# Optimization experiments

Measured on AMD Instinct MI355X. Metric: run time of the kernel, lower is better.

## Reference

```python
import jax, jax.numpy as jnp
import numpy as np
import math

D_MODEL = 1024
NUM_HEADS = 16
D_K = D_MODEL // NUM_HEADS
SEQ = 4096
THETA = 10000.0


def _rope_tables(d_k, max_seq_len, theta):
    freqs = 1.0 / theta ** (jnp.arange(0, d_k, 2, dtype=jnp.float32) / d_k)  # (d_k/2,)
    pos = jnp.arange(max_seq_len, dtype=jnp.float32)
    ang = pos[:, None] * freqs[None, :]  # (S, d_k/2)
    return jnp.cos(ang), jnp.sin(ang)


def setup_inputs() -> dict:
    key = jax.random.key(0)
    ks = jax.random.split(key, 5)
    std = math.sqrt(2.0 / (D_MODEL + D_MODEL))
    def trunc_w(k):
        return jax.random.truncated_normal(k, -3.0, 3.0, (D_MODEL, D_MODEL), jnp.float32) * std
    x = jax.random.normal(ks[0], (1, SEQ, D_MODEL), jnp.float32)
    Wq, Wk, Wv, Wo = trunc_w(ks[1]), trunc_w(ks[2]), trunc_w(ks[3]), trunc_w(ks[4])
    cos, sin = _rope_tables(D_K, SEQ, THETA)
    positions = jnp.arange(SEQ, dtype=jnp.int32)
    return {"x": x, "Wq": Wq, "Wk": Wk, "Wv": Wv, "Wo": Wo,
            "cos": cos, "sin": sin, "positions": positions}


def _apply_rope(t, cos, sin, positions):
    # t: (b, h, s, d_k); cos/sin: (max_s, d_k/2)
    c = cos[positions][None, None]  # (1,1,s,d_k/2)
    s = sin[positions][None, None]
    x1, x2 = t[..., ::2], t[..., 1::2]
    rotated = jnp.stack([x1 * c - x2 * s, x1 * s + x2 * c], axis=-1)  # (b,h,s,d_k/2,2)
    return rotated.reshape(t.shape)


def reference(x, Wq, Wk, Wv, Wo, cos, sin, positions):
    b, s, d = x.shape
    h, dk = NUM_HEADS, D_K
    def proj(W):
        y = jnp.einsum('bsi,oi->bso', x, W)
        return y.reshape(b, s, h, dk).transpose(0, 2, 1, 3)  # (b,h,s,dk)
    Q, K, V = proj(Wq), proj(Wk), proj(Wv)
    Q = _apply_rope(Q, cos, sin, positions)
    K = _apply_rope(K, cos, sin, positions)
    scores = jnp.einsum('bhqd,bhkd->bhqk', Q, K) / math.sqrt(dk)
    causal = jnp.tril(jnp.ones((s, s), dtype=bool))
    scores = jnp.where(causal[None, None], scores, -jnp.inf)
    weights = jax.nn.softmax(scores, axis=-1)
    y = jnp.einsum('bhqk,bhkd->bhqd', weights, V)
    y = y.transpose(0, 2, 1, 3).reshape(b, s, d)
    return jnp.einsum('bsi,oi->bso', y, Wo)
```

## Files before the change

### kernel.cpp

```cpp
#include <hip/hip_runtime.h>
#include <math.h>

#define SEQ 4096
#define DM  1024
#define NH  16
#define DK  64

typedef __attribute__((ext_vector_type(4))) float f32x4;
typedef __attribute__((ext_vector_type(8))) short bf16x8;
typedef __attribute__((ext_vector_type(8))) unsigned short u16x8;

__device__ __forceinline__ unsigned short bf_hi(float f) {
    return (unsigned short)(__float_as_uint(f) >> 16);
}
__device__ __forceinline__ float bf_f(unsigned short s) {
    return __uint_as_float(((unsigned)s) << 16);
}

union FragU { u16x8 u; bf16x8 b; ushort4 q[2]; };

template<int MODE>
__global__ __launch_bounds__(256)
void gemm_mfma(const float* __restrict__ A,
               const float* __restrict__ W0, const float* __restrict__ W1,
               const float* __restrict__ W2,
               unsigned short* __restrict__ OQh, unsigned short* __restrict__ OQl,
               unsigned short* __restrict__ OKh, unsigned short* __restrict__ OKl,
               unsigned short* __restrict__ OVh, unsigned short* __restrict__ OVl,
               float* __restrict__ Ofp,
               const float* __restrict__ cosT, const float* __restrict__ sinT,
               const int* __restrict__ positions)
{
    constexpr int NT = (MODE == 4) ? 48 : 16;
    __shared__ unsigned short As[128][72];
    __shared__ unsigned short Bs[64][72];

    const int t   = threadIdx.x;
    const int bid = blockIdx.x;
    const int q8  = (32 * NT) >> 3;
    const int swz = (bid & 7) * q8 + (bid >> 3);
    const int by  = swz / NT;
    const int bxf = swz % NT;
    const int wt  = (MODE == 4) ? (bxf >> 4) : 0;
    const int bx  = (MODE == 4) ? (bxf & 15) : bxf;
    const int m0  = by * 128;
    const int n0  = bx * 64;
    const float* W = (MODE == 4) ? (wt == 0 ? W0 : (wt == 1 ? W1 : W2)) : W0;

    const int lane = t & 63;
    const int w    = t >> 6;
    const int wr   = w >> 1, wc = w & 1;
    const int l15  = lane & 15;
    const int lg   = lane >> 4;

    const int ar = t >> 1, ah = t & 1;
    const int br = t >> 2, bq = t & 3;
    const float* Ap = &A[(size_t)(m0 + ar) * DM + ah * 16];
    const float* Wp = &W[(size_t)(n0 + br) * DM + bq * 8];

    f32x4 acc[4][2];
#pragma unroll
    for (int mi = 0; mi < 4; ++mi)
#pragma unroll
        for (int ni = 0; ni < 2; ++ni) acc[mi][ni] = (f32x4){0.f, 0.f, 0.f, 0.f};

    float4 pa[4], pb[2];
#pragma unroll
    for (int u = 0; u < 4; ++u) pa[u] = *reinterpret_cast<const float4*>(Ap + u * 4);
    pb[0] = *reinterpret_cast<const float4*>(Wp);
    pb[1] = *reinterpret_cast<const float4*>(Wp + 4);

    for (int kt = 0; kt < 32; ++kt) {
#pragma unroll
        for (int g = 0; g < 4; ++g) {
            ushort4 hv, lv;
            const float4 v = pa[g];
            const float vf[4] = {v.x, v.y, v.z, v.w};
            unsigned short* hp = (unsigned short*)&hv;
            unsigned short* lp = (unsigned short*)&lv;
#pragma unroll
            for (int jj = 0; jj < 4; ++jj) {
                const unsigned short h = bf_hi(vf[jj]);
                hp[jj] = h; lp[jj] = bf_hi(vf[jj] - bf_f(h));
            }
            *reinterpret_cast<ushort4*>(&As[ar][8 * g + 4 * ah])      = hv;
            *reinterpret_cast<ushort4*>(&As[ar][32 + 8 * g + 4 * ah]) = lv;
        }
#pragma unroll
        for (int u = 0; u < 2; ++u) {
            const int g = 2 * (bq & 1) + u, h2 = bq >> 1;
            ushort4 hv, lv;
            const float4 v = pb[u];
            const float vf[4] = {v.x, v.y, v.z, v.w};
            unsigned short* hp = (unsigned short*)&hv;
            unsigned short* lp = (unsigned short*)&lv;
#pragma unroll
            for (int jj = 0; jj < 4; ++jj) {
                const unsigned short h = bf_hi(vf[jj]);
                hp[jj] = h; lp[jj] = bf_hi(vf[jj] - bf_f(h));
            }
            *reinterpret_cast<ushort4*>(&Bs[br][8 * g + 4 * h2])      = hv;
            *reinterpret_cast<ushort4*>(&Bs[br][32 + 8 * g + 4 * h2]) = lv;
        }
        __syncthreads();

        if (kt < 31) {
            const float* Apn = Ap + (kt + 1) * 32;
            const float* Wpn = Wp + (kt + 1) * 32;
#pragma unroll
            for (int u = 0; u < 4; ++u) pa[u] = *reinterpret_cast<const float4*>(Apn + u * 4);
            pb[0] = *reinterpret_cast<const float4*>(Wpn);
            pb[1] = *reinterpret_cast<const float4*>(Wpn + 4);
        }

        FragU a_h[4], a_l[4], b_h[2], b_l[2];
#pragma unroll
        for (int mi = 0; mi < 4; ++mi) {
            const int row = wr * 64 + mi * 16 + l15;
            a_h[mi].u = *reinterpret_cast<const u16x8*>(&As[row][8 * lg]);
            a_l[mi].u = *reinterpret_cast<const u16x8*>(&As[row][32 + 8 * lg]);
        }
#pragma unroll
        for (int ni = 0; ni < 2; ++ni) {
            const int row = wc * 32 + ni * 16 + l15;
            b_h[ni].u = *reinterpret_cast<const u16x8*>(&Bs[row][8 * lg]);
            b_l[ni].u = *reinterpret_cast<const u16x8*>(&Bs[row][32 + 8 * lg]);
        }
#pragma unroll
        for (int mi = 0; mi < 4; ++mi)
#pragma unroll
            for (int ni = 0; ni < 2; ++ni) {
                f32x4 c = acc[mi][ni];
                c = __builtin_amdgcn_mfma_f32_16x16x32_bf16(a_h[mi].b, b_h[ni].b, c, 0, 0, 0);
                c = __builtin_amdgcn_mfma_f32_16x16x32_bf16(a_h[mi].b, b_l[ni].b, c, 0, 0, 0);
                c = __builtin_amdgcn_mfma_f32_16x16x32_bf16(a_l[mi].b, b_h[ni].b, c, 0, 0, 0);
                acc[mi][ni] = c;
            }
        __syncthreads();
    }

    if (MODE == 0) {
#pragma unroll
        for (int mi = 0; mi < 4; ++mi)
#pragma unroll
            for (int ni = 0; ni < 2; ++ni)
#pragma unroll
                for (int r = 0; r < 4; ++r) {
                    const int m  = m0 + wr * 64 + mi * 16 + lg * 4 + r;
                    const int ng = n0 + wc * 32 + ni * 16 + l15;
                    Ofp[(size_t)m * DM + ng] = acc[mi][ni][r];
                }
    } else if (wt == 2) {
#pragma unroll
        for (int mi = 0; mi < 4; ++mi)
#pragma unroll
            for (int ni = 0; ni < 2; ++ni) {
                ushort4 hv, lv;
                unsigned short* hp = (unsigned short*)&hv;
                unsigned short* lp = (unsigned short*)&lv;
#pragma unroll
                for (int r = 0; r < 4; ++r) {
                    const float f = acc[mi][ni][r];
                    const unsigned short h = bf_hi(f);
                    hp[r] = h; lp[r] = bf_hi(f - bf_f(h));
                }
                const int ng = n0 + wc * 32 + ni * 16 + l15;
                const size_t off = (size_t)ng * SEQ + m0 + wr * 64 + mi * 16 + lg * 4;
                *reinterpret_cast<ushort4*>(&OVh[off]) = hv;
                *reinterpret_cast<ushort4*>(&OVl[off]) = lv;
            }
    } else {
        unsigned short* Oh = (wt == 0) ? OQh : OKh;
        unsigned short* Ol = (wt == 0) ? OQl : OKl;
        const int head = bx;
#pragma unroll
        for (int mi = 0; mi < 4; ++mi)
#pragma unroll
            for (int r = 0; r < 4; ++r) {
                const int m   = m0 + wr * 64 + mi * 16 + lg * 4 + r;
                const int pos = positions[m];
#pragma unroll
                for (int ni = 0; ni < 2; ++ni) {
                    float val = acc[mi][ni][r];
                    const int d = wc * 32 + ni * 16 + l15;
                    const float other = __shfl_xor(val, 1);
                    const float cc = cosT[pos * (DK / 2) + (d >> 1)];
                    const float ss = sinT[pos * (DK / 2) + (d >> 1)];
                    val = (d & 1) ? fmaf(other, ss, val * cc)
                                  : fmaf(other, -ss, val * cc);
                    if (wt == 0) val *= 0.125f;
                    const unsigned short h = bf_hi(val);
                    const unsigned short l = bf_hi(val - bf_f(h));
                    const size_t off = ((size_t)head * SEQ + m) * DK + d;
                    Oh[off] = h; Ol[off] = l;
                }
            }
    }
}

__global__ __launch_bounds__(256)
void attn_mfma(const unsigned short* __restrict__ Qhi, const unsigned short* __restrict__ Qlo,
               const unsigned short* __restrict__ Khi, const unsigned short* __restrict__ Klo,
               const unsigned short* __restrict__ Vhi, const unsigned short* __restrict__ Vlo,
               float* __restrict__ Y)
{
    __shared__ unsigned short KsH[64][68], KsL[64][68];
    __shared__ unsigned short VsH[64][68], VsL[64][68];

    const int t    = threadIdx.x;
    const int lane = t & 63;
    const int w    = t >> 6;
    const int bid  = blockIdx.x;
    const int h    = 2 * (bid & 7) + ((bid >> 3) >> 5);
    const int bx   = (bid >> 3) & 31;

    const int l15 = lane & 15;
    const int lg  = lane >> 4;
    const int dg  = lg * 4;

#pragma unroll 1
    for (int pass = 0; pass < 2; ++pass) {
        const int qt = pass ? (63 - bx) : bx;

        bf16x8 qh[2], ql[2];
        {
            const size_t qrow = ((size_t)h * SEQ + (size_t)qt * 64 + w * 16 + l15) * DK;
#pragma unroll
            for (int c = 0; c < 2; ++c) {
                FragU uh, ul;
                uh.q[0] = *reinterpret_cast<const ushort4*>(&Qhi[qrow + c * 32 + dg]);
                uh.q[1] = *reinterpret_cast<const ushort4*>(&Qhi[qrow + c * 32 + 16 + dg]);
                ul.q[0] = *reinterpret_cast<const ushort4*>(&Qlo[qrow + c * 32 + dg]);
                ul.q[1] = *reinterpret_cast<const ushort4*>(&Qlo[qrow + c * 32 + 16 + dg]);
                qh[c] = uh.b; ql[c] = ul.b;
            }
        }

        f32x4 yacc[4];
#pragma unroll
        for (int dt = 0; dt < 4; ++dt) yacc[dt] = (f32x4){0.f, 0.f, 0.f, 0.f};
        float m_run = -1e30f, l_run = 0.0f;

        for (int kt = 0; kt <= qt; ++kt) {
            __syncthreads();
            {
                const int srow = t >> 3;
                const int scol = (t & 7) * 8;
#pragma unroll
                for (int u = 0; u < 2; ++u) {
                    const int row = u * 32 + srow;
                    const size_t gK = ((size_t)h * SEQ + (size_t)kt * 64 + row) * DK + scol;
                    const size_t gV = ((size_t)h * DK + row) * SEQ + (size_t)kt * 64 + scol;
                    FragU a;
                    a.u = *reinterpret_cast<const u16x8*>(&Khi[gK]);
                    *reinterpret_cast<ushort4*>(&KsH[row][scol])     = a.q[0];
                    *reinterpret_cast<ushort4*>(&KsH[row][scol + 4]) = a.q[1];
                    a.u = *reinterpret_cast<const u16x8*>(&Klo[gK]);
                    *reinterpret_cast<ushort4*>(&KsL[row][scol])     = a.q[0];
                    *reinterpret_cast<ushort4*>(&KsL[row][scol + 4]) = a.q[1];
                    a.u = *reinterpret_cast<const u16x8*>(&Vhi[gV]);
                    *reinterpret_cast<ushort4*>(&VsH[row][scol])     = a.q[0];
                    *reinterpret_cast<ushort4*>(&VsH[row][scol + 4]) = a.q[1];
                    a.u = *reinterpret_cast<const u16x8*>(&Vlo[gV]);
                    *reinterpret_cast<ushort4*>(&VsL[row][scol])     = a.q[0];
                    *reinterpret_cast<ushort4*>(&VsL[row][scol + 4]) = a.q[1];
                }
            }
            __syncthreads();

            const bool diag = (kt == qt);

            f32x4 st[4];
            __builtin_amdgcn_s_setprio(1);
#pragma unroll
            for (int ktile = 0; ktile < 4; ++ktile) {
                if (diag && ktile > w) {
                    st[ktile] = (f32x4){-1e30f, -1e30f, -1e30f, -1e30f};
                    continue;
                }
                f32x4 s = (f32x4){0.f, 0.f, 0.f, 0.f};
#pragma unroll
                for (int c = 0; c < 2; ++c) {
                    const int d0 = c * 32 + dg;
                    FragU ahf, alf;
                    ahf.q[0] = *reinterpret_cast<const ushort4*>(&KsH[ktile * 16 + l15][d0]);
                    ahf.q[1] = *reinterpret_cast<const ushort4*>(&KsH[ktile * 16 + l15][d0 + 16]);
                    alf.q[0] = *reinterpret_cast<const ushort4*>(&KsL[ktile * 16 + l15][d0]);
                    alf.q[1] = *reinterpret_cast<const ushort4*>(&KsL[ktile * 16 + l15][d0 + 16]);
                    s = __builtin_amdgcn_mfma_f32_16x16x32_bf16(ahf.b, qh[c], s, 0, 0, 0);
                    s = __builtin_amdgcn_mfma_f32_16x16x32_bf16(ahf.b, ql[c], s, 0, 0, 0);
                    s = __builtin_amdgcn_mfma_f32_16x16x32_bf16(alf.b, qh[c], s, 0, 0, 0);
                }
                st[ktile] = s;
            }
            __builtin_amdgcn_s_setprio(0);

            if (diag) {
                const int qrel = w * 16 + l15;
#pragma unroll
                for (int ktile = 0; ktile < 4; ++ktile)
#pragma unroll
                    for (int r = 0; r < 4; ++r)
                        if (ktile * 16 + dg + r > qrel) st[ktile][r] = -1e30f;
            }

            float rowmax = -1e30f;
#pragma unroll
            for (int ktile = 0; ktile < 4; ++ktile)
#pragma unroll
                for (int r = 0; r < 4; ++r) rowmax = fmaxf(rowmax, st[ktile][r]);
            rowmax = fmaxf(rowmax, __shfl_xor(rowmax, 16));
            rowmax = fmaxf(rowmax, __shfl_xor(rowmax, 32));
            if (!__all(rowmax <= m_run + 8.0f)) {
                const float mnew   = fmaxf(m_run, rowmax);
                const float factor = __expf(m_run - mnew);
                l_run *= factor;
#pragma unroll
                for (int r = 0; r < 4; ++r) {
                    const float fr = __shfl(factor, (lg << 2) | r);
#pragma unroll
                    for (int dt = 0; dt < 4; ++dt) yacc[dt][r] *= fr;
                }
                m_run = mnew;
            }

            float psum = 0.0f;
            unsigned short ph[4][4], pl[4][4];
#pragma unroll
            for (int ktile = 0; ktile < 4; ++ktile)
#pragma unroll
                for (int r = 0; r < 4; ++r) {
                    const float p = __expf(st[ktile][r] - m_run);
                    psum += p;
                    const unsigned short hh = bf_hi(p);
                    ph[ktile][r] = hh;
                    pl[ktile][r] = bf_hi(p - bf_f(hh));
                }
            psum += __shfl_xor(psum, 16);
            psum += __shfl_xor(psum, 32);
            l_run += psum;

            union { unsigned short a[8]; bf16x8 v; } pah[2], pal[2];
#pragma unroll
            for (int c = 0; c < 2; ++c)
#pragma unroll
                for (int j = 0; j < 4; ++j) {
                    pah[c].a[j]     = ph[2 * c][j];
                    pah[c].a[4 + j] = ph[2 * c + 1][j];
                    pal[c].a[j]     = pl[2 * c][j];
                    pal[c].a[4 + j] = pl[2 * c + 1][j];
                }

            const int cmax = diag ? (w >> 1) : 1;
            __builtin_amdgcn_s_setprio(1);
#pragma unroll
            for (int dt = 0; dt < 4; ++dt) {
                f32x4 acc = yacc[dt];
#pragma unroll
                for (int c = 0; c < 2; ++c) {
                    if (c > cmax) break;
                    const int k0 = c * 32 + dg;
                    FragU vh, vl;
                    vh.q[0] = *reinterpret_cast<const ushort4*>(&VsH[dt * 16 + l15][k0]);
                    vh.q[1] = *reinterpret_cast<const ushort4*>(&VsH[dt * 16 + l15][k0 + 16]);
                    vl.q[0] = *reinterpret_cast<const ushort4*>(&VsL[dt * 16 + l15][k0]);
                    vl.q[1] = *reinterpret_cast<const ushort4*>(&VsL[dt * 16 + l15][k0 + 16]);
                    acc = __builtin_amdgcn_mfma_f32_16x16x32_bf16(pah[c].v, vh.b, acc, 0, 0, 0);
                    acc = __builtin_amdgcn_mfma_f32_16x16x32_bf16(pah[c].v, vl.b, acc, 0, 0, 0);
                    acc = __builtin_amdgcn_mfma_f32_16x16x32_bf16(pal[c].v, vh.b, acc, 0, 0, 0);
                }
                yacc[dt] = acc;
            }
            __builtin_amdgcn_s_setprio(0);
        }

        const float inv = 1.0f / l_run;
#pragma unroll
        for (int r = 0; r < 4; ++r) {
            const float ir = __shfl(inv, (lg << 2) | r);
            float* yp = &Y[((size_t)qt * 64 + w * 16 + lg * 4 + r) * DM + h * DK];
#pragma unroll
            for (int dt = 0; dt < 4; ++dt) yp[dt * 16 + l15] = yacc[dt][r] * ir;
        }
    }
}

extern "C" void kernel_launch(void* const* d_in, const int* in_sizes, int n_in,
                              void* d_out, int out_size, void* d_ws, size_t ws_size,
                              hipStream_t stream)
{
    const float* x    = (const float*)d_in[0];
    const float* Wq   = (const float*)d_in[1];
    const float* Wk   = (const float*)d_in[2];
    const float* Wv   = (const float*)d_in[3];
    const float* Wo   = (const float*)d_in[4];
    const float* cosT = (const float*)d_in[5];
    const float* sinT = (const float*)d_in[6];
    const int*   pos  = (const int*)d_in[7];
    float* out = (float*)d_out;

    const size_t E = (size_t)SEQ * DM;
    unsigned short* qh = (unsigned short*)d_ws;
    unsigned short* ql = qh + E;
    unsigned short* kh = ql + E;
    unsigned short* kl = kh + E;
    unsigned short* vh = kl + E;
    unsigned short* vl = vh + E;
    float* y = (float*)(vl + E);

    gemm_mfma<4><<<dim3(32 * 48), dim3(256), 0, stream>>>(
        x, Wq, Wk, Wv, qh, ql, kh, kl, vh, vl, nullptr, cosT, sinT, pos);
    attn_mfma<<<dim3(512), dim3(256), 0, stream>>>(qh, ql, kh, kl, vh, vl, y);
    gemm_mfma<0><<<dim3(32 * 16), dim3(256), 0, stream>>>(
        y, Wo, nullptr, nullptr, nullptr, nullptr, nullptr, nullptr, nullptr, nullptr,
        out, cosT, sinT, pos);
}
```

Baseline: 287.9 us.

## Enlarge GEMM tiles, process two query tiles per attention block, use hardware bf16 packing

The GEMM tile grows from 128x64 to 128x128 with launch_bounds occupancy hints, and attention output is written as bf16 hi/lo pairs, so the output projection no longer re-splits fp32 data. Attention handles 128 query rows per block. It folds log2(e) into the Q scale so v_exp_f32 can be used directly, widens the rescale threshold, and drops the low-precision P term in the PV product. Packing now uses v_cvt_pk_bf16_f32 (round-to-nearest) instead of truncation. These changes aim to raise MFMA reuse and cut conversion ALU work, but they increase register pressure and reduce P precision.

```diff
diff --git a/kernel.cpp b/kernel.cpp
--- a/kernel.cpp
+++ b/kernel.cpp
@@ -10,18 +10,35 @@
 typedef __attribute__((ext_vector_type(8))) short bf16x8;
 typedef __attribute__((ext_vector_type(8))) unsigned short u16x8;
 
-__device__ __forceinline__ unsigned short bf_hi(float f) {
-    return (unsigned short)(__float_as_uint(f) >> 16);
-}
-__device__ __forceinline__ float bf_f(unsigned short s) {
-    return __uint_as_float(((unsigned)s) << 16);
-}
-
-union FragU { u16x8 u; bf16x8 b; ushort4 q[2]; };
+union FragU { u16x8 u; bf16x8 b; ushort4 q[2]; unsigned w[4]; };
+
+__device__ __forceinline__ unsigned cvtpk(float a, float b) {
+    unsigned r; asm("v_cvt_pk_bf16_f32 %0, %1, %2" : "=v"(r) : "v"(a), "v"(b)); return r;
+}
+__device__ __forceinline__ float fexp2(float x) {
+    float r; asm("v_exp_f32 %0, %1" : "=v"(r) : "v"(x)); return r;
+}
+__device__ __forceinline__ void split4(float4 v, ushort4& hv, ushort4& lv) {
+    union { ushort4 q; unsigned w[2]; } H, L;
+    H.w[0] = cvtpk(v.x, v.y); H.w[1] = cvtpk(v.z, v.w);
+    const float rx = v.x - __uint_as_float(H.w[0] << 16);
+    const float ry = v.y - __uint_as_float(H.w[0] & 0xffff0000u);
+    const float rz = v.z - __uint_as_float(H.w[1] << 16);
+    const float rw = v.w - __uint_as_float(H.w[1] & 0xffff0000u);
+    L.w[0] = cvtpk(rx, ry); L.w[1] = cvtpk(rz, rw);
+    hv = H.q; lv = L.q;
+}
+__device__ __forceinline__ void split1(float f, unsigned short& h, unsigned short& l) {
+    const unsigned hw = cvtpk(f, f) & 0xffffu;
+    h = (unsigned short)hw;
+    const float r = f - __uint_as_float(hw << 16);
+    l = (unsigned short)(__float_as_uint(r) >> 16);
+}
 
 template<int MODE>
-__global__ __launch_bounds__(256)
-void gemm_mfma(const float* __restrict__ A,
+__global__ __launch_bounds__(256, 2)
+void gemm_mfma(const float* __restrict__ Af,
+               const unsigned short* __restrict__ Ahi, const unsigned short* __restrict__ Alo,
                const float* __restrict__ W0, const float* __restrict__ W1,
                const float* __restrict__ W2,
                unsigned short* __restrict__ OQh, unsigned short* __restrict__ OQl,
@@ -31,148 +48,154 @@
                const float* __restrict__ cosT, const float* __restrict__ sinT,
                const int* __restrict__ positions)
 {
-    constexpr int NT = (MODE == 4) ? 48 : 16;
-    __shared__ unsigned short As[128][72];
-    __shared__ unsigned short Bs[64][72];
+    constexpr int NT = (MODE == 4) ? 24 : 8;
+    __shared__ unsigned short As[128][76];
+    __shared__ unsigned short Bs[128][76];
 
     const int t   = threadIdx.x;
     const int bid = blockIdx.x;
-    const int q8  = (32 * NT) >> 3;
-    const int swz = (bid & 7) * q8 + (bid >> 3);
+    const int qpx = (32 * NT) >> 3;
+    const int swz = (bid & 7) * qpx + (bid >> 3);
     const int by  = swz / NT;
     const int bxf = swz % NT;
-    const int wt  = (MODE == 4) ? (bxf >> 4) : 0;
-    const int bx  = (MODE == 4) ? (bxf & 15) : bxf;
+    const int wt  = (MODE == 4) ? (bxf >> 3) : 0;
+    const int bx  = (MODE == 4) ? (bxf & 7) : bxf;
     const int m0  = by * 128;
-    const int n0  = bx * 64;
     const float* W = (MODE == 4) ? (wt == 0 ? W0 : (wt == 1 ? W1 : W2)) : W0;
 
-    const int lane = t & 63;
-    const int w    = t >> 6;
-    const int wr   = w >> 1, wc = w & 1;
-    const int l15  = lane & 15;
-    const int lg   = lane >> 4;
+    const int lane = t & 63, w = t >> 6;
+    const int wr = w >> 1, wc = w & 1;
+    const int l15 = lane & 15, lg = lane >> 4;
 
     const int ar = t >> 1, ah = t & 1;
-    const int br = t >> 2, bq = t & 3;
-    const float* Ap = &A[(size_t)(m0 + ar) * DM + ah * 16];
-    const float* Wp = &W[(size_t)(n0 + br) * DM + bq * 8];
-
-    f32x4 acc[4][2];
+    const float* Ap = (MODE == 4) ? &Af[(size_t)(m0 + ar) * DM + ah * 16] : nullptr;
+    const unsigned short* Aph = (MODE == 0) ? &Ahi[(size_t)(m0 + ar) * DM + ah * 16] : nullptr;
+    const unsigned short* Apl = (MODE == 0) ? &Alo[(size_t)(m0 + ar) * DM + ah * 16] : nullptr;
+    const float* Wp = &W[(size_t)(bx * 128 + ar) * DM + ah * 16];
+
+    f32x4 acc[4][4];
 #pragma unroll
     for (int mi = 0; mi < 4; ++mi)
 #pragma unroll
-        for (int ni = 0; ni < 2; ++ni) acc[mi][ni] = (f32x4){0.f, 0.f, 0.f, 0.f};
-
-    float4 pa[4], pb[2];
-#pragma unroll
-    for (int u = 0; u < 4; ++u) pa[u] = *reinterpret_cast<const float4*>(Ap + u * 4);
-    pb[0] = *reinterpret_cast<const float4*>(Wp);
-    pb[1] = *reinterpret_cast<const float4*>(Wp + 4);
+        for (int ni = 0; ni < 4; ++ni) acc[mi][ni] = (f32x4){0.f, 0.f, 0.f, 0.f};
+
+    float4 pa[4], pb[4];
+    u16x8 pah[2], pal[2];
+    if constexpr (MODE == 4) {
+#pragma unroll
+        for (int g = 0; g < 4; ++g) pa[g] = *reinterpret_cast<const float4*>(Ap + g * 4);
+    } else {
+        pah[0] = *reinterpret_cast<const u16x8*>(Aph);
+        pah[1] = *reinterpret_cast<const u16x8*>(Aph + 8);
+        pal[0] = *reinterpret_cast<const u16x8*>(Apl);
+        pal[1] = *reinterpret_cast<const u16x8*>(Apl + 8);
+    }
+#pragma unroll
+    for (int g = 0; g < 4; ++g) pb[g] = *reinterpret_cast<const float4*>(Wp + g * 4);
 
     for (int kt = 0; kt < 32; ++kt) {
+        if constexpr (MODE == 4) {
+#pragma unroll
+            for (int g = 0; g < 4; ++g) {
+                ushort4 hv, lv;
+                split4(pa[g], hv, lv);
+                *reinterpret_cast<ushort4*>(&As[ar][8 * g + 4 * ah])      = hv;
+                *reinterpret_cast<ushort4*>(&As[ar][32 + 8 * g + 4 * ah]) = lv;
+            }
+        } else {
+            FragU h0, h1, l0, l1;
+            h0.u = pah[0]; h1.u = pah[1]; l0.u = pal[0]; l1.u = pal[1];
+            *reinterpret_cast<ushort4*>(&As[ar][0  + 4 * ah]) = h0.q[0];
+            *reinterpret_cast<ushort4*>(&As[ar][8  + 4 * ah]) = h0.q[1];
+            *reinterpret_cast<ushort4*>(&As[ar][16 + 4 * ah]) = h1.q[0];
+            *reinterpret_cast<ushort4*>(&As[ar][24 + 4 * ah]) = h1.q[1];
+            *reinterpret_cast<ushort4*>(&As[ar][32 + 4 * ah]) = l0.q[0];
+            *reinterpret_cast<ushort4*>(&As[ar][40 + 4 * ah]) = l0.q[1];
+            *reinterpret_cast<ushort4*>(&As[ar][48 + 4 * ah]) = l1.q[0];
+            *reinterpret_cast<ushort4*>(&As[ar][56 + 4 * ah]) = l1.q[1];
+        }
 #pragma unroll
         for (int g = 0; g < 4; ++g) {
             ushort4 hv, lv;
-            const float4 v = pa[g];
-            const float vf[4] = {v.x, v.y, v.z, v.w};
-            unsigned short* hp = (unsigned short*)&hv;
-            unsigned short* lp = (unsigned short*)&lv;
-#pragma unroll
-            for (int jj = 0; jj < 4; ++jj) {
-                const unsigned short h = bf_hi(vf[jj]);
-                hp[jj] = h; lp[jj] = bf_hi(vf[jj] - bf_f(h));
-            }
-            *reinterpret_cast<ushort4*>(&As[ar][8 * g + 4 * ah])      = hv;
-            *reinterpret_cast<ushort4*>(&As[ar][32 + 8 * g + 4 * ah]) = lv;
-        }
-#pragma unroll
-        for (int u = 0; u < 2; ++u) {
-            const int g = 2 * (bq & 1) + u, h2 = bq >> 1;
-            ushort4 hv, lv;
-            const float4 v = pb[u];
-            const float vf[4] = {v.x, v.y, v.z, v.w};
-            unsigned short* hp = (unsigned short*)&hv;
-            unsigned short* lp = (unsigned short*)&lv;
-#pragma unroll
-            for (int jj = 0; jj < 4; ++jj) {
-                const unsigned short h = bf_hi(vf[jj]);
-                hp[jj] = h; lp[jj] = bf_hi(vf[jj] - bf_f(h));
-            }
-            *reinterpret_cast<ushort4*>(&Bs[br][8 * g + 4 * h2])      = hv;
-            *reinterpret_cast<ushort4*>(&Bs[br][32 + 8 * g + 4 * h2]) = lv;
+            split4(pb[g], hv, lv);
+            *reinterpret_cast<ushort4*>(&Bs[ar][8 * g + 4 * ah])      = hv;
+            *reinterpret_cast<ushort4*>(&Bs[ar][32 + 8 * g + 4 * ah]) = lv;
         }
         __syncthreads();
 
         if (kt < 31) {
-            const float* Apn = Ap + (kt + 1) * 32;
-            const float* Wpn = Wp + (kt + 1) * 32;
-#pragma unroll
-            for (int u = 0; u < 4; ++u) pa[u] = *reinterpret_cast<const float4*>(Apn + u * 4);
-            pb[0] = *reinterpret_cast<const float4*>(Wpn);
-            pb[1] = *reinterpret_cast<const float4*>(Wpn + 4);
-        }
-
-        FragU a_h[4], a_l[4], b_h[2], b_l[2];
-#pragma unroll
-        for (int mi = 0; mi < 4; ++mi) {
-            const int row = wr * 64 + mi * 16 + l15;
-            a_h[mi].u = *reinterpret_cast<const u16x8*>(&As[row][8 * lg]);
-            a_l[mi].u = *reinterpret_cast<const u16x8*>(&As[row][32 + 8 * lg]);
-        }
-#pragma unroll
-        for (int ni = 0; ni < 2; ++ni) {
-            const int row = wc * 32 + ni * 16 + l15;
+            const int ko = (kt + 1) * 32;
+            if constexpr (MODE == 4) {
+#pragma unroll
+                for (int g = 0; g < 4; ++g)
+                    pa[g] = *reinterpret_cast<const float4*>(Ap + ko + g * 4);
+            } else {
+                pah[0] = *reinterpret_cast<const u16x8*>(Aph + ko);
+                pah[1] = *reinterpret_cast<const u16x8*>(Aph + ko + 8);
+                pal[0] = *reinterpret_cast<const u16x8*>(Apl + ko);
+                pal[1] = *reinterpret_cast<const u16x8*>(Apl + ko + 8);
+            }
+#pragma unroll
+            for (int g = 0; g < 4; ++g)
+                pb[g] = *reinterpret_cast<const float4*>(Wp + ko + g * 4);
+        }
+
+        FragU b_h[4], b_l[4];
+#pragma unroll
+        for (int ni = 0; ni < 4; ++ni) {
+            const int row = wc * 64 + ni * 16 + l15;
             b_h[ni].u = *reinterpret_cast<const u16x8*>(&Bs[row][8 * lg]);
             b_l[ni].u = *reinterpret_cast<const u16x8*>(&Bs[row][32 + 8 * lg]);
         }
 #pragma unroll
-        for (int mi = 0; mi < 4; ++mi)
-#pragma unroll
-            for (int ni = 0; ni < 2; ++ni) {
+        for (int mi = 0; mi < 4; ++mi) {
+            FragU a_h, a_l;
+            const int row = wr * 64 + mi * 16 + l15;
+            a_h.u = *reinterpret_cast<const u16x8*>(&As[row][8 * lg]);
+            a_l.u = *reinterpret_cast<const u16x8*>(&As[row][32 + 8 * lg]);
+#pragma unroll
+            for (int ni = 0; ni < 4; ++ni) {
                 f32x4 c = acc[mi][ni];
-                c = __builtin_amdgcn_mfma_f32_16x16x32_bf16(a_h[mi].b, b_h[ni].b, c, 0, 0, 0);
-                c = __builtin_amdgcn_mfma_f32_16x16x32_bf16(a_h[mi].b, b_l[ni].b, c, 0, 0, 0);
-                c = __builtin_amdgcn_mfma_f32_16x16x32_bf16(a_l[mi].b, b_h[ni].b, c, 0, 0, 0);
+                c = __builtin_amdgcn_mfma_f32_16x16x32_bf16(a_h.b, b_h[ni].b, c, 0, 0, 0);
+                c = __builtin_amdgcn_mfma_f32_16x16x32_bf16(a_h.b, b_l[ni].b, c, 0, 0, 0);
+                c = __builtin_amdgcn_mfma_f32_16x16x32_bf16(a_l.b, b_h[ni].b, c, 0, 0, 0);
                 acc[mi][ni] = c;
             }
+        }
         __syncthreads();
     }
 
-    if (MODE == 0) {
+    if constexpr (MODE == 0) {
 #pragma unroll
         for (int mi = 0; mi < 4; ++mi)
 #pragma unroll
-            for (int ni = 0; ni < 2; ++ni)
+            for (int ni = 0; ni < 4; ++ni)
 #pragma unroll
                 for (int r = 0; r < 4; ++r) {
-                    const int m  = m0 + wr * 64 + mi * 16 + lg * 4 + r;
-                    const int ng = n0 + wc * 32 + ni * 16 + l15;
-                    Ofp[(size_t)m * DM + ng] = acc[mi][ni][r];
+                    const int m = m0 + wr * 64 + mi * 16 + lg * 4 + r;
+                    const int n = bx * 128 + wc * 64 + ni * 16 + l15;
+                    Ofp[(size_t)m * DM + n] = acc[mi][ni][r];
                 }
     } else if (wt == 2) {
 #pragma unroll
         for (int mi = 0; mi < 4; ++mi)
 #pragma unroll
-            for (int ni = 0; ni < 2; ++ni) {
+            for (int ni = 0; ni < 4; ++ni) {
                 ushort4 hv, lv;
                 unsigned short* hp = (unsigned short*)&hv;
                 unsigned short* lp = (unsigned short*)&lv;
 #pragma unroll
-                for (int r = 0; r < 4; ++r) {
-                    const float f = acc[mi][ni][r];
-                    const unsigned short h = bf_hi(f);
-                    hp[r] = h; lp[r] = bf_hi(f - bf_f(h));
-                }
-                const int ng = n0 + wc * 32 + ni * 16 + l15;
-                const size_t off = (size_t)ng * SEQ + m0 + wr * 64 + mi * 16 + lg * 4;
+                for (int r = 0; r < 4; ++r) split1(acc[mi][ni][r], hp[r], lp[r]);
+                const int vrow = bx * 128 + wc * 64 + ni * 16 + l15;
+                const size_t off = (size_t)vrow * SEQ + m0 + wr * 64 + mi * 16 + lg * 4;
                 *reinterpret_cast<ushort4*>(&OVh[off]) = hv;
                 *reinterpret_cast<ushort4*>(&OVl[off]) = lv;
             }
     } else {
         unsigned short* Oh = (wt == 0) ? OQh : OKh;
         unsigned short* Ol = (wt == 0) ? OQl : OKl;
-        const int head = bx;
+        const int head = bx * 2 + wc;
+        const float qsc = 0.1803368801f;
 #pragma unroll
         for (int mi = 0; mi < 4; ++mi)
 #pragma unroll
@@ -180,51 +203,54 @@
                 const int m   = m0 + wr * 64 + mi * 16 + lg * 4 + r;
                 const int pos = positions[m];
 #pragma unroll
-                for (int ni = 0; ni < 2; ++ni) {
+                for (int ni = 0; ni < 4; ++ni) {
                     float val = acc[mi][ni][r];
-                    const int d = wc * 32 + ni * 16 + l15;
+                    const int d = ni * 16 + l15;
                     const float other = __shfl_xor(val, 1);
-                    const float cc = cosT[pos * (DK / 2) + (d >> 1)];
-                    const float ss = sinT[pos * (DK / 2) + (d >> 1)];
+                    const float cc = cosT[pos * 32 + ni * 8 + (l15 >> 1)];
+                    const float ss = sinT[pos * 32 + ni * 8 + (l15 >> 1)];
                     val = (d & 1) ? fmaf(other, ss, val * cc)
                                   : fmaf(other, -ss, val * cc);
-                    if (wt == 0) val *= 0.125f;
-                    const unsigned short h = bf_hi(val);
-                    const unsigned short l = bf_hi(val - bf_f(h));
+                    if (wt == 0) val *= qsc;
+                    unsigned short hh, ll;
+                    split1(val, hh, ll);
                     const size_t off = ((size_t)head * SEQ + m) * DK + d;
-                    Oh[off] = h; Ol[off] = l;
+                    Oh[off] = hh; Ol[off] = ll;
                 }
             }
     }
 }
 
-__global__ __launch_bounds__(256)
+__global__ __launch_bounds__(256, 1)
 void attn_mfma(const unsigned short* __restrict__ Qhi, const unsigned short* __restrict__ Qlo,
                const unsigned short* __restrict__ Khi, const unsigned short* __restrict__ Klo,
                const unsigned short* __restrict__ Vhi, const unsigned short* __restrict__ Vlo,
-               float* __restrict__ Y)
+               unsigned short* __restrict__ Yh, unsigned short* __restrict__ Yl)
 {
-    __shared__ unsigned short KsH[64][68], KsL[64][68];
-    __shared__ unsigned short VsH[64][68], VsL[64][68];
-
-    const int t    = threadIdx.x;
-    const int lane = t & 63;
-    const int w    = t >> 6;
-    const int bid  = blockIdx.x;
-    const int h    = 2 * (bid & 7) + ((bid >> 3) >> 5);
-    const int bx   = (bid >> 3) & 31;
-
-    const int l15 = lane & 15;
-    const int lg  = lane >> 4;
-    const int dg  = lg * 4;
+    __shared__ unsigned short KsH[64][72], KsL[64][72];
+    __shared__ unsigned short VsH[64][72], VsL[64][72];
+
+    const int t = threadIdx.x, lane = t & 63, w = t >> 6;
+    const int bid = blockIdx.x;
+    const int xcd = bid & 7, idx = bid >> 3;
+    const int h = 2 * xcd + (idx >> 4);
+    const int pairI = idx & 15;
+    const int l15 = lane & 15, lg = lane >> 4, dg = lg * 4;
+    const int srow = t >> 2, q16 = t & 3;
+    const int sc0 = (q16 >> 1) * 32 + 4 * (q16 & 1);
+
+    u16x8 pf[8];
 
 #pragma unroll 1
     for (int pass = 0; pass < 2; ++pass) {
-        const int qt = pass ? (63 - bx) : bx;
-
-        bf16x8 qh[2], ql[2];
-        {
-            const size_t qrow = ((size_t)h * SEQ + (size_t)qt * 64 + w * 16 + l15) * DK;
+        const int qt = pass ? (31 - pairI) : pairI;
+        const int K0 = 2 * qt;
+        const int ktmax = K0 + 1;
+
+        bf16x8 qh[2][2], ql[2][2];
+#pragma unroll
+        for (int u = 0; u < 2; ++u) {
+            const size_t qrow = ((size_t)h * SEQ + (size_t)qt * 128 + u * 64 + w * 16 + l15) * DK;
 #pragma unroll
             for (int c = 0; c < 2; ++c) {
                 FragU uh, ul;
@@ -232,155 +258,196 @@
                 uh.q[1] = *reinterpret_cast<const ushort4*>(&Qhi[qrow + c * 32 + 16 + dg]);
                 ul.q[0] = *reinterpret_cast<const ushort4*>(&Qlo[qrow + c * 32 + dg]);
                 ul.q[1] = *reinterpret_cast<const ushort4*>(&Qlo[qrow + c * 32 + 16 + dg]);
-                qh[c] = uh.b; ql[c] = ul.b;
-            }
-        }
-
-        f32x4 yacc[4];
-#pragma unroll
-        for (int dt = 0; dt < 4; ++dt) yacc[dt] = (f32x4){0.f, 0.f, 0.f, 0.f};
-        float m_run = -1e30f, l_run = 0.0f;
-
-        for (int kt = 0; kt <= qt; ++kt) {
+                qh[u][c] = uh.b; ql[u][c] = ul.b;
+            }
+        }
+
+        f32x4 yacc[2][4];
+#pragma unroll
+        for (int u = 0; u < 2; ++u)
+#pragma unroll
+            for (int dt = 0; dt < 4; ++dt) yacc[u][dt] = (f32x4){0.f, 0.f, 0.f, 0.f};
+        float m_run[2] = {-1e30f, -1e30f}, l_run[2] = {0.f, 0.f};
+
+        {
+            const size_t gK = ((size_t)h * SEQ + srow) * DK + q16 * 16;
+            const size_t gV = ((size_t)h * DK + srow) * SEQ + q16 * 16;
+            pf[0] = *reinterpret_cast<const u16x8*>(&Khi[gK]);
+            pf[1] = *reinterpret_cast<const u16x8*>(&Khi[gK + 8]);
+            pf[2] = *reinterpret_cast<const u16x8*>(&Klo[gK]);
+            pf[3] = *reinterpret_cast<const u16x8*>(&Klo[gK + 8]);
+            pf[4] = *reinterpret_cast<const u16x8*>(&Vhi[gV]);
+            pf[5] = *reinterpret_cast<const u16x8*>(&Vhi[gV + 8]);
+            pf[6] = *reinterpret_cast<const u16x8*>(&Vlo[gV]);
+            pf[7] = *reinterpret_cast<const u16x8*>(&Vlo[gV + 8]);
+        }
+
+        for (int kt = 0; kt <= ktmax; ++kt) {
             __syncthreads();
             {
-                const int srow = t >> 3;
-                const int scol = (t & 7) * 8;
-#pragma unroll
-                for (int u = 0; u < 2; ++u) {
-                    const int row = u * 32 + srow;
-                    const size_t gK = ((size_t)h * SEQ + (size_t)kt * 64 + row) * DK + scol;
-                    const size_t gV = ((size_t)h * DK + row) * SEQ + (size_t)kt * 64 + scol;
-                    FragU a;
-                    a.u = *reinterpret_cast<const u16x8*>(&Khi[gK]);
-                    *reinterpret_cast<ushort4*>(&KsH[row][scol])     = a.q[0];
-                    *reinterpret_cast<ushort4*>(&KsH[row][scol + 4]) = a.q[1];
-                    a.u = *reinterpret_cast<const u16x8*>(&Klo[gK]);
-                    *reinterpret_cast<ushort4*>(&KsL[row][scol])     = a.q[0];
-                    *reinterpret_cast<ushort4*>(&KsL[row][scol + 4]) = a.q[1];
-                    a.u = *reinterpret_cast<const u16x8*>(&Vhi[gV]);
-                    *reinterpret_cast<ushort4*>(&VsH[row][scol])     = a.q[0];
-                    *reinterpret_cast<ushort4*>(&VsH[row][scol + 4]) = a.q[1];
-                    a.u = *reinterpret_cast<const u16x8*>(&Vlo[gV]);
-                    *reinterpret_cast<ushort4*>(&VsL[row][scol])     = a.q[0];
-                    *reinterpret_cast<ushort4*>(&VsL[row][scol + 4]) = a.q[1];
-                }
+                FragU f0, f1;
+                f0.u = pf[0]; f1.u = pf[1];
+                *reinterpret_cast<ushort4*>(&KsH[srow][sc0])      = f0.q[0];
+                *reinterpret_cast<ushort4*>(&KsH[srow][sc0 + 8])  = f0.q[1];
+                *reinterpret_cast<ushort4*>(&KsH[srow][sc0 + 16]) = f1.q[0];
+                *reinterpret_cast<ushort4*>(&KsH[srow][sc0 + 24]) = f1.q[1];
+                f0.u = pf[2]; f1.u = pf[3];
+                *reinterpret_cast<ushort4*>(&KsL[srow][sc0])      = f0.q[0];
+                *reinterpret_cast<ushort4*>(&KsL[srow][sc0 + 8])  = f0.q[1];
+                *reinterpret_cast<ushort4*>(&KsL[srow][sc0 + 16]) = f1.q[0];
+                *reinterpret_cast<ushort4*>(&KsL[srow][sc0 + 24]) = f1.q[1];
+                f0.u = pf[4]; f1.u = pf[5];
+                *reinterpret_cast<ushort4*>(&VsH[srow][sc0])      = f0.q[0];
+                *reinterpret_cast<ushort4*>(&VsH[srow][sc0 + 8])  = f0.q[1];
+                *reinterpret_cast<ushort4*>(&VsH[srow][sc0 + 16]) = f1.q[0];
+                *reinterpret_cast<ushort4*>(&VsH[srow][sc0 + 24]) = f1.q[1];
+                f0.u = pf[6]; f1.u = pf[7];
+                *reinterpret_cast<ushort4*>(&VsL[srow][sc0])      = f0.q[0];
+                *reinterpret_cast<ushort4*>(&VsL[srow][sc0 + 8])  = f0.q[1];
+                *reinterpret_cast<ushort4*>(&VsL[srow][sc0 + 16]) = f1.q[0];
+                *reinterpret_cast<ushort4*>(&VsL[srow][sc0 + 24]) = f1.q[1];
             }
             __syncthreads();
 
-            const bool diag = (kt == qt);
-
-            f32x4 st[4];
-            __builtin_amdgcn_s_setprio(1);
+            if (kt < ktmax) {
+                const size_t gK = ((size_t)h * SEQ + (size_t)(kt + 1) * 64 + srow) * DK + q16 * 16;
+                const size_t gV = ((size_t)h * DK + srow) * SEQ + (size_t)(kt + 1) * 64 + q16 * 16;
+                pf[0] = *reinterpret_cast<const u16x8*>(&Khi[gK]);
+                pf[1] = *reinterpret_cast<const u16x8*>(&Khi[gK + 8]);
+                pf[2] = *reinterpret_cast<const u16x8*>(&Klo[gK]);
+                pf[3] = *reinterpret_cast<const u16x8*>(&Klo[gK + 8]);
+                pf[4] = *reinterpret_cast<const u16x8*>(&Vhi[gV]);
+                pf[5] = *reinterpret_cast<const u16x8*>(&Vhi[gV + 8]);
+                pf[6] = *reinterpret_cast<const u16x8*>(&Vlo[gV]);
+                pf[7] = *reinterpret_cast<const u16x8*>(&Vlo[gV + 8]);
+            }
+
+            const int mode0 = (kt < K0) ? 1 : ((kt == K0) ? 2 : 0);
+            const int mode1 = (kt <= K0) ? 1 : 2;
+            const bool act0 = (mode0 != 0);
+
+            f32x4 st0[4], st1[4];
 #pragma unroll
             for (int ktile = 0; ktile < 4; ++ktile) {
-                if (diag && ktile > w) {
-                    st[ktile] = (f32x4){-1e30f, -1e30f, -1e30f, -1e30f};
-                    continue;
-                }
-                f32x4 s = (f32x4){0.f, 0.f, 0.f, 0.f};
+                const bool sk0 = !act0 || (mode0 == 2 && ktile > w);
+                const bool sk1 = (mode1 == 2 && ktile > w);
+                f32x4 s0 = (f32x4){0.f, 0.f, 0.f, 0.f};
+                f32x4 s1 = (f32x4){0.f, 0.f, 0.f, 0.f};
+                if (!sk0 || !sk1) {
+#pragma unroll
+                    for (int c = 0; c < 2; ++c) {
+                        FragU kh, kl;
+                        kh.u = *reinterpret_cast<const u16x8*>(&KsH[ktile * 16 + l15][c * 32 + 8 * lg]);
+                        kl.u = *reinterpret_cast<const u16x8*>(&KsL[ktile * 16 + l15][c * 32 + 8 * lg]);
+                        if (!sk0) {
+                            s0 = __builtin_amdgcn_mfma_f32_16x16x32_bf16(kh.b, qh[0][c], s0, 0, 0, 0);
+                            s0 = __builtin_amdgcn_mfma_f32_16x16x32_bf16(kh.b, ql[0][c], s0, 0, 0, 0);
+                            s0 = __builtin_amdgcn_mfma_f32_16x16x32_bf16(kl.b, qh[0][c], s0, 0, 0, 0);
+                        }
+                        if (!sk1) {
+                            s1 = __builtin_amdgcn_mfma_f32_16x16x32_bf16(kh.b, qh[1][c], s1, 0, 0, 0);
+                            s1 = __builtin_amdgcn_mfma_f32_16x16x32_bf16(kh.b, ql[1][c], s1, 0, 0, 0);
+                            s1 = __builtin_amdgcn_mfma_f32_16x16x32_bf16(kl.b, qh[1][c], s1, 0, 0, 0);
+                        }
+                    }
+                }
+                st0[ktile] = sk0 ? (f32x4){-1e30f, -1e30f, -1e30f, -1e30f} : s0;
+                st1[ktile] = sk1 ? (f32x4){-1e30f, -1e30f, -1e30f, -1e30f} : s1;
+            }
+
+            if (mode0 == 2) {
+#pragma unroll
+                for (int ktile = 0; ktile < 4; ++ktile)
+#pragma unroll
+                    for (int r = 0; r < 4; ++r)
+                        if (ktile * 16 + dg + r > w * 16 + l15) st0[ktile][r] = -1e30f;
+            }
+            if (mode1 == 2) {
+#pragma unroll
+                for (int ktile = 0; ktile < 4; ++ktile)
+#pragma unroll
+                    for (int r = 0; r < 4; ++r)
+                        if (ktile * 16 + dg + r > w * 16 + l15) st1[ktile][r] = -1e30f;
+            }
+
+            bf16x8 pa0[2], pa1[2];
+#pragma unroll
+            for (int u = 0; u < 2; ++u) {
+                if (u == 0 && !act0) continue;
+                f32x4* st = (u == 0) ? st0 : st1;
+                float rowmax = st[0][0];
+#pragma unroll
+                for (int ktile = 0; ktile < 4; ++ktile)
+#pragma unroll
+                    for (int r = 0; r < 4; ++r) rowmax = fmaxf(rowmax, st[ktile][r]);
+                rowmax = fmaxf(rowmax, __shfl_xor(rowmax, 16));
+                rowmax = fmaxf(rowmax, __shfl_xor(rowmax, 32));
+                if (!__all(rowmax <= m_run[u] + 11.5f)) {
+                    const float mnew = fmaxf(m_run[u], rowmax);
+                    const float factor = fexp2(m_run[u] - mnew);
+                    l_run[u] *= factor;
+#pragma unroll
+                    for (int r = 0; r < 4; ++r) {
+                        const float fr = __shfl(factor, (lg << 2) | r);
+#pragma unroll
+                        for (int dt = 0; dt < 4; ++dt) yacc[u][dt][r] *= fr;
+                    }
+                    m_run[u] = mnew;
+                }
+                float p[4][4]; float psum = 0.f;
+#pragma unroll
+                for (int ktile = 0; ktile < 4; ++ktile)
+#pragma unroll
+                    for (int r = 0; r < 4; ++r) {
+                        p[ktile][r] = fexp2(st[ktile][r] - m_run[u]);
+                        psum += p[ktile][r];
+                    }
+                psum += __shfl_xor(psum, 16);
+                psum += __shfl_xor(psum, 32);
+                l_run[u] += psum;
 #pragma unroll
                 for (int c = 0; c < 2; ++c) {
-                    const int d0 = c * 32 + dg;
-                    FragU ahf, alf;
-                    ahf.q[0] = *reinterpret_cast<const ushort4*>(&KsH[ktile * 16 + l15][d0]);
-                    ahf.q[1] = *reinterpret_cast<const ushort4*>(&KsH[ktile * 16 + l15][d0 + 16]);
-                    alf.q[0] = *reinterpret_cast<const ushort4*>(&KsL[ktile * 16 + l15][d0]);
-                    alf.q[1] = *reinterpret_cast<const ushort4*>(&KsL[ktile * 16 + l15][d0 + 16]);
-                    s = __builtin_amdgcn_mfma_f32_16x16x32_bf16(ahf.b, qh[c], s, 0, 0, 0);
-                    s = __builtin_amdgcn_mfma_f32_16x16x32_bf16(ahf.b, ql[c], s, 0, 0, 0);
-                    s = __builtin_amdgcn_mfma_f32_16x16x32_bf16(alf.b, qh[c], s, 0, 0, 0);
-                }
-                st[ktile] = s;
-            }
-            __builtin_amdgcn_s_setprio(0);
-
-            if (diag) {
-                const int qrel = w * 16 + l15;
-#pragma unroll
-                for (int ktile = 0; ktile < 4; ++ktile)
-#pragma unroll
-                    for (int r = 0; r < 4; ++r)
-                        if (ktile * 16 + dg + r > qrel) st[ktile][r] = -1e30f;
-            }
-
-            float rowmax = -1e30f;
-#pragma unroll
-            for (int ktile = 0; ktile < 4; ++ktile)
-#pragma unroll
-                for (int r = 0; r < 4; ++r) rowmax = fmaxf(rowmax, st[ktile][r]);
-            rowmax = fmaxf(rowmax, __shfl_xor(rowmax, 16));
-            rowmax = fmaxf(rowmax, __shfl_xor(rowmax, 32));
-            if (!__all(rowmax <= m_run + 8.0f)) {
-                const float mnew   = fmaxf(m_run, rowmax);
-                const float factor = __expf(m_run - mnew);
-                l_run *= factor;
-#pragma unroll
-                for (int r = 0; r < 4; ++r) {
-                    const float fr = __shfl(factor, (lg << 2) | r);
-#pragma unroll
-                    for (int dt = 0; dt < 4; ++dt) yacc[dt][r] *= fr;
-                }
-                m_run = mnew;
-            }
-
-            float psum = 0.0f;
-            unsigned short ph[4][4], pl[4][4];
-#pragma unroll
-            for (int ktile = 0; ktile < 4; ++ktile)
-#pragma unroll
-                for (int r = 0; r < 4; ++r) {
-                    const float p = __expf(st[ktile][r] - m_run);
-                    psum += p;
-                    const unsigned short hh = bf_hi(p);
-                    ph[ktile][r] = hh;
-                    pl[ktile][r] = bf_hi(p - bf_f(hh));
-                }
-            psum += __shfl_xor(psum, 16);
-            psum += __shfl_xor(psum, 32);
-            l_run += psum;
-
-            union { unsigned short a[8]; bf16x8 v; } pah[2], pal[2];
-#pragma unroll
-            for (int c = 0; c < 2; ++c)
-#pragma unroll
-                for (int j = 0; j < 4; ++j) {
-                    pah[c].a[j]     = ph[2 * c][j];
-                    pah[c].a[4 + j] = ph[2 * c + 1][j];
-                    pal[c].a[j]     = pl[2 * c][j];
-                    pal[c].a[4 + j] = pl[2 * c + 1][j];
-                }
-
-            const int cmax = diag ? (w >> 1) : 1;
-            __builtin_amdgcn_s_setprio(1);
+                    FragU P;
+                    P.w[0] = cvtpk(p[2 * c][0],     p[2 * c][1]);
+                    P.w[1] = cvtpk(p[2 * c][2],     p[2 * c][3]);
+                    P.w[2] = cvtpk(p[2 * c + 1][0], p[2 * c + 1][1]);
+                    P.w[3] = cvtpk(p[2 * c + 1][2], p[2 * c + 1][3]);
+                    if (u == 0) pa0[c] = P.b; else pa1[c] = P.b;
+                }
+            }
+
 #pragma unroll
             for (int dt = 0; dt < 4; ++dt) {
-                f32x4 acc = yacc[dt];
 #pragma unroll
                 for (int c = 0; c < 2; ++c) {
-                    if (c > cmax) break;
-                    const int k0 = c * 32 + dg;
                     FragU vh, vl;
-                    vh.q[0] = *reinterpret_cast<const ushort4*>(&VsH[dt * 16 + l15][k0]);
-                    vh.q[1] = *reinterpret_cast<const ushort4*>(&VsH[dt * 16 + l15][k0 + 16]);
-                    vl.q[0] = *reinterpret_cast<const ushort4*>(&VsL[dt * 16 + l15][k0]);
-                    vl.q[1] = *reinterpret_cast<const ushort4*>(&VsL[dt * 16 + l15][k0 + 16]);
-                    acc = __builtin_amdgcn_mfma_f32_16x16x32_bf16(pah[c].v, vh.b, acc, 0, 0, 0);
-                    acc = __builtin_amdgcn_mfma_f32_16x16x32_bf16(pah[c].v, vl.b, acc, 0, 0, 0);
-                    acc = __builtin_amdgcn_mfma_f32_16x16x32_bf16(pal[c].v, vh.b, acc, 0, 0, 0);
-                }
-                yacc[dt] = acc;
-            }
-            __builtin_amdgcn_s_setprio(0);
-        }
-
-        const float inv = 1.0f / l_run;
-#pragma unroll
-        for (int r = 0; r < 4; ++r) {
-            const float ir = __shfl(inv, (lg << 2) | r);
-            float* yp = &Y[((size_t)qt * 64 + w * 16 + lg * 4 + r) * DM + h * DK];
-#pragma unroll
-            for (int dt = 0; dt < 4; ++dt) yp[dt * 16 + l15] = yacc[dt][r] * ir;
+                    vh.u = *reinterpret_cast<const u16x8*>(&VsH[dt * 16 + l15][c * 32 + 8 * lg]);
+                    vl.u = *reinterpret_cast<const u16x8*>(&VsL[dt * 16 + l15][c * 32 + 8 * lg]);
+                    if (act0) {
+                        yacc[0][dt] = __builtin_amdgcn_mfma_f32_16x16x32_bf16(pa0[c], vh.b, yacc[0][dt], 0, 0, 0);
+                        yacc[0][dt] = __builtin_amdgcn_mfma_f32_16x16x32_bf16(pa0[c], vl.b, yacc[0][dt], 0, 0, 0);
+                    }
+                    yacc[1][dt] = __builtin_amdgcn_mfma_f32_16x16x32_bf16(pa1[c], vh.b, yacc[1][dt], 0, 0, 0);
+                    yacc[1][dt] = __builtin_amdgcn_mfma_f32_16x16x32_bf16(pa1[c], vl.b, yacc[1][dt], 0, 0, 0);
+                }
+            }
+        }
+
+#pragma unroll
+        for (int u = 0; u < 2; ++u) {
+            const float inv = 1.0f / l_run[u];
+#pragma unroll
+            for (int r = 0; r < 4; ++r) {
+                const float ir = __shfl(inv, (lg << 2) | r);
+                const size_t row = (size_t)qt * 128 + u * 64 + w * 16 + lg * 4 + r;
+#pragma unroll
+                for (int dt = 0; dt < 4; ++dt) {
+                    unsigned short hh, ll;
+                    split1(yacc[u][dt][r] * ir, hh, ll);
+                    const size_t off = row * DM + h * DK + dt * 16 + l15;
+                    Yh[off] = hh; Yl[off] = ll;
+                }
+            }
         }
     }
 }
@@ -406,12 +473,14 @@
     unsigned short* kl = kh + E;
     unsigned short* vh = kl + E;
     unsigned short* vl = vh + E;
-    float* y = (float*)(vl + E);
-
-    gemm_mfma<4><<<dim3(32 * 48), dim3(256), 0, stream>>>(
-        x, Wq, Wk, Wv, qh, ql, kh, kl, vh, vl, nullptr, cosT, sinT, pos);
-    attn_mfma<<<dim3(512), dim3(256), 0, stream>>>(qh, ql, kh, kl, vh, vl, y);
-    gemm_mfma<0><<<dim3(32 * 16), dim3(256), 0, stream>>>(
-        y, Wo, nullptr, nullptr, nullptr, nullptr, nullptr, nullptr, nullptr, nullptr,
-        out, cosT, sinT, pos);
-}
+    unsigned short* yh = vl + E;
+    unsigned short* yl = yh + E;
+
+    gemm_mfma<4><<<dim3(768), dim3(256), 0, stream>>>(
+        x, nullptr, nullptr, Wq, Wk, Wv,
+        qh, ql, kh, kl, vh, vl, nullptr, cosT, sinT, pos);
+    attn_mfma<<<dim3(256), dim3(256), 0, stream>>>(qh, ql, kh, kl, vh, vl, yh, yl);
+    gemm_mfma<0><<<dim3(256), dim3(256), 0, stream>>>(
+        nullptr, yh, yl, Wo, nullptr, nullptr,
+        nullptr, nullptr, nullptr, nullptr, nullptr, nullptr, out, cosT, sinT, pos);
+}
```

Result: faster. 258.9 us (-10.1%).
